# Kernel tuning notes

Measured on AMD Instinct MI355X. Metric: run time of the kernel, lower is better.

The kernel has to match this reference:

```python
import jax, jax.numpy as jnp
import numpy as np

D_MODEL = 1024
NHEAD = 16
HEAD_DIM = D_MODEL // NHEAD


def setup_inputs() -> dict:
    key = jax.random.key(0)
    ks = jax.random.split(key, 9)
    B, T = 2, 2048
    s = 1.0 / np.sqrt(D_MODEL)
    return {
        "sequence": jax.random.normal(ks[0], (B, T, D_MODEL), dtype=jnp.float32),
        "wq": jax.random.normal(ks[1], (D_MODEL, D_MODEL), dtype=jnp.float32) * s,
        "bq": jax.random.normal(ks[2], (D_MODEL,), dtype=jnp.float32) * 0.01,
        "wk": jax.random.normal(ks[3], (D_MODEL, D_MODEL), dtype=jnp.float32) * s,
        "bk": jax.random.normal(ks[4], (D_MODEL,), dtype=jnp.float32) * 0.01,
        "wv": jax.random.normal(ks[5], (D_MODEL, D_MODEL), dtype=jnp.float32) * s,
        "bv": jax.random.normal(ks[6], (D_MODEL,), dtype=jnp.float32) * 0.01,
        "wo": jax.random.normal(ks[7], (D_MODEL, D_MODEL), dtype=jnp.float32) * s,
        "bo": jax.random.normal(ks[8], (D_MODEL,), dtype=jnp.float32) * 0.01,
    }


def reference(sequence, wq, bq, wk, bk, wv, bv, wo, bo):
    B, T, C = sequence.shape
    scale = jnp.asarray(HEAD_DIM ** 0.5, sequence.dtype)
    # projections (nn.Linear: x @ W.T + b)
    def proj(x, w, b):
        y = x @ w.T + b
        return y.reshape(B, T, NHEAD, HEAD_DIM).transpose(0, 2, 1, 3)  # [B,H,T,Dh]
    q = proj(sequence, wq, bq)
    k = proj(sequence, wk, bk)
    v = proj(sequence, wv, bv)
    scores = jnp.einsum("bhqd,bhkd->bhqk", q, k) / scale
    causal = jnp.tril(jnp.ones((T, T), dtype=bool))
    scores = jnp.where(causal, scores, jnp.asarray(-jnp.inf, scores.dtype))
    attn = jax.nn.softmax(scores, axis=-1)
    out = jnp.einsum("bhqk,bhkd->bhqd", attn, v)
    out = out.transpose(0, 2, 1, 3).reshape(B, T, C)
    return out @ wo.T + bo
```

## Files before the change

### kernel.cpp

```cpp
#include <hip/hip_runtime.h>
#include <hip/hip_bf16.h>
#include <hip/hip_fp16.h>
#include <type_traits>

#define DM 1024
#define NH 16
#define HD 64
#define BATCH 2
#define SEQ 2048
#define MROWS (BATCH*SEQ)

typedef __hip_bfloat16 bf16;
typedef __attribute__((ext_vector_type(8))) short    bf16x8;
typedef __attribute__((ext_vector_type(8))) short    s16x8;
typedef __attribute__((ext_vector_type(8))) _Float16 f16x8;
typedef __attribute__((ext_vector_type(4))) _Float16 f16x4;
typedef __attribute__((ext_vector_type(4))) short    s16x4;
typedef __attribute__((ext_vector_type(4))) float    f32x4;

#define LOG2E 1.44269504f
#define M_FIX 4.0f

__device__ __forceinline__ short f2bf(float x) {
    union { float f; unsigned u; } v; v.f = x;
    unsigned r = v.u + 0x7FFF + ((v.u >> 16) & 1);
    return (short)(r >> 16);
}

__device__ __forceinline__ bf16x8 ld8f(const float* p) {
    const float4 a = *(const float4*)p;
    const float4 b = *(const float4*)(p + 4);
    bf16x8 r;
    r[0]=f2bf(a.x); r[1]=f2bf(a.y); r[2]=f2bf(a.z); r[3]=f2bf(a.w);
    r[4]=f2bf(b.x); r[5]=f2bf(b.y); r[6]=f2bf(b.z); r[7]=f2bf(b.w);
    return r;
}

__device__ __forceinline__ void gload_lds16(const void* g, void* l) {
    __builtin_amdgcn_global_load_lds(
        (const __attribute__((address_space(1))) void*)g,
        (__attribute__((address_space(3))) void*)l, 16, 0, 0);
}

__global__ __launch_bounds__(256)
void cvt_bf16(const float* __restrict__ s0, const float* __restrict__ s1,
              const float* __restrict__ s2, const float* __restrict__ s3,
              const float* __restrict__ s4,
              short* d0, short* d1, short* d2, short* d3, short* d4)
{
    const int y = blockIdx.y;
    const float* src = (y==0? s0 : y==1? s1 : y==2? s2 : y==3? s3 : s4);
    short*       dst = (y==0? d0 : y==1? d1 : y==2? d2 : y==3? d3 : d4);
    const int n = (y == 0) ? MROWS*DM : DM*DM;
    const int i = (blockIdx.x * 256 + threadIdx.x) * 8;
    if (i < n) *(bf16x8*)(dst + i) = ld8f(src + i);
}

template<int MODE>
__device__ __forceinline__
void gemm_epilogue(f32x4 (&acc)[4][4], const float* bi, void* out, int z,
                   int tile_m, int tile_n, int wm, int wn,
                   int fr, int quad, int lane, short* lA)
{
    if (MODE == 1 && z == 2) {
        __syncthreads();
        short* sc = lA + (int)(threadIdx.x >> 6) * 256;
        const int rd = lane >> 2, tc = lane & 3;
        #pragma unroll
        for (int mi = 0; mi < 4; ++mi) {
            #pragma unroll
            for (int ni = 0; ni < 4; ++ni) {
                const int colg = tile_n + wn + ni*16 + fr;
                const float bia = bi[colg];
                f16x4 w;
                #pragma unroll
                for (int r = 0; r < 4; ++r) w[r] = (_Float16)(acc[mi][ni][r] + bia);
                *(f16x4*)(sc + fr*16 + quad*4) = w;
                const f16x4 vv = *(const f16x4*)(sc + rd*16 + tc*4);
                const int dg = tile_n + wn + ni*16 + rd;
                const int tg = tile_m + wm + mi*16 + tc*4;
                const int hh = dg >> 6, dd = dg & (HD-1);
                const int bb = tg >> 11, tt = tg & (SEQ-1);
                const int kt = tt >> 5, tko = tt & 31;
                *(f16x4*)((_Float16*)out +
                    ((((size_t)(bb*NH + hh))*(SEQ/32) + kt)*HD + dd)*32 + tko) = vv;
            }
        }
    } else {
        #pragma unroll
        for (int mi = 0; mi < 4; ++mi) {
            #pragma unroll
            for (int ni = 0; ni < 4; ++ni) {
                const int colg = tile_n + wn + ni*16 + fr;
                const float bia = bi[colg];
                #pragma unroll
                for (int r = 0; r < 4; ++r) {
                    const int rowg = tile_m + wm + mi*16 + quad*4 + r;
                    const float v = acc[mi][ni][r] + bia;
                    if (MODE == 0) {
                        ((float*)out)[(size_t)rowg*DM + colg] = v;
                    } else {
                        const int bb = rowg >> 11, t = rowg & (SEQ-1);
                        const int h  = colg >> 6,  d = colg & (HD-1);
                        ((_Float16*)out)[(((size_t)(bb*NH + h))*SEQ + t)*HD + d] = (_Float16)v;
                    }
                }
            }
        }
    }
}

template<int MODE>
__global__ __launch_bounds__(256)
void gemm_a(const short* __restrict__ A,
            const short* __restrict__ W0, const short* __restrict__ W1, const short* __restrict__ W2,
            const float* __restrict__ b0, const float* __restrict__ b1, const float* __restrict__ b2,
            void* o0, void* o1, void* o2)
{
    __shared__ __align__(16) short lA[128*32];
    __shared__ __align__(16) short lB[128*32];

    const int tid  = threadIdx.x;
    const int wid  = tid >> 6;
    const int lane = tid & 63;
    const int tile_n = blockIdx.x * 128;
    const int tile_m = blockIdx.y * 128;
    const int z = blockIdx.z;

    const short* Wg = (z == 0 ? W0 : (z == 1 ? W1 : W2));
    const float* bi = (z == 0 ? b0 : (z == 1 ? b1 : b2));
    void*        out = (z == 0 ? o0 : (z == 1 ? o1 : o2));

    const int sa_row = tile_m + wid*32 + (lane >> 2);
    const int sb_row = tile_n + wid*32 + (lane >> 2);
    const int scol   = (lane & 3) * 8;
    short* lA0 = lA + wid*1024 + lane*8;
    short* lA1 = lA0 + 512;
    short* lB0 = lB + wid*1024 + lane*8;
    short* lB1 = lB0 + 512;

    const int wm = (wid >> 1) * 64;
    const int wn = (wid & 1) * 64;
    const int fr = lane & 15;
    const int quad = lane >> 4;
    const int fq = quad * 8;

    f32x4 acc[4][4] = {};

    for (int k0 = 0; k0 < DM; k0 += 32) {
        __syncthreads();
        gload_lds16(A  + (size_t)sa_row*DM      + k0 + scol, lA0);
        gload_lds16(A  + (size_t)(sa_row+16)*DM + k0 + scol, lA1);
        gload_lds16(Wg + (size_t)sb_row*DM      + k0 + scol, lB0);
        gload_lds16(Wg + (size_t)(sb_row+16)*DM + k0 + scol, lB1);
        __syncthreads();

        bf16x8 af[4], bfv[4];
        #pragma unroll
        for (int i = 0; i < 4; ++i) af[i]  = *(const bf16x8*)(lA + (wm + i*16 + fr)*32 + fq);
        #pragma unroll
        for (int i = 0; i < 4; ++i) bfv[i] = *(const bf16x8*)(lB + (wn + i*16 + fr)*32 + fq);

        #pragma unroll
        for (int mi = 0; mi < 4; ++mi)
            #pragma unroll
            for (int ni = 0; ni < 4; ++ni)
                acc[mi][ni] = __builtin_amdgcn_mfma_f32_16x16x32_bf16(
                    af[mi], bfv[ni], acc[mi][ni], 0, 0, 0);
    }
    gemm_epilogue<MODE>(acc, bi, out, z, tile_m, tile_n, wm, wn, fr, quad, lane, lA);
}

template<typename TA, int MODE>
__global__ __launch_bounds__(256)
void gemm_f(const TA* __restrict__ A,
            const float* __restrict__ W0, const float* __restrict__ W1, const float* __restrict__ W2,
            const float* __restrict__ b0, const float* __restrict__ b1, const float* __restrict__ b2,
            void* o0, void* o1, void* o2)
{
    __shared__ __align__(16) short lA[128*32];
    __shared__ __align__(16) short lB[128*32];

    const int tid  = threadIdx.x;
    const int wid  = tid >> 6;
    const int lane = tid & 63;
    const int tile_n = blockIdx.x * 128;
    const int tile_m = blockIdx.y * 128;
    const int z = blockIdx.z;

    const float* Wg = (z == 0 ? W0 : (z == 1 ? W1 : W2));
    const float* bi = (z == 0 ? b0 : (z == 1 ? b1 : b2));
    void*        out = (z == 0 ? o0 : (z == 1 ? o1 : o2));

    const int sa_row = tile_m + wid*32 + (lane >> 2);
    const int sb_row = tile_n + wid*32 + (lane >> 2);
    const int scol   = (lane & 3) * 8;
    short* lA0 = lA + wid*1024 + lane*8;
    short* lA1 = lA0 + 512;
    short* lB0 = lB + wid*1024 + lane*8;
    short* lB1 = lB0 + 512;

    const int wm = (wid >> 1) * 64;
    const int wn = (wid & 1) * 64;
    const int fr = lane & 15;
    const int quad = lane >> 4;
    const int fq = quad * 8;

    f32x4 acc[4][4] = {};

    for (int k0 = 0; k0 < DM; k0 += 32) {
        bf16x8 ra0, ra1;
        if constexpr (std::is_same<TA, float>::value) {
            ra0 = ld8f((const float*)A + (size_t)sa_row*DM      + k0 + scol);
            ra1 = ld8f((const float*)A + (size_t)(sa_row+16)*DM + k0 + scol);
        } else {
            ra0 = *(const bf16x8*)((const short*)A + (size_t)sa_row*DM      + k0 + scol);
            ra1 = *(const bf16x8*)((const short*)A + (size_t)(sa_row+16)*DM + k0 + scol);
        }
        const bf16x8 rb0 = ld8f(Wg + (size_t)sb_row*DM      + k0 + scol);
        const bf16x8 rb1 = ld8f(Wg + (size_t)(sb_row+16)*DM + k0 + scol);

        __syncthreads();
        *(bf16x8*)lA0 = ra0;
        *(bf16x8*)lA1 = ra1;
        *(bf16x8*)lB0 = rb0;
        *(bf16x8*)lB1 = rb1;
        __syncthreads();

        bf16x8 af[4], bfv[4];
        #pragma unroll
        for (int i = 0; i < 4; ++i) af[i]  = *(const bf16x8*)(lA + (wm + i*16 + fr)*32 + fq);
        #pragma unroll
        for (int i = 0; i < 4; ++i) bfv[i] = *(const bf16x8*)(lB + (wn + i*16 + fr)*32 + fq);

        #pragma unroll
        for (int mi = 0; mi < 4; ++mi)
            #pragma unroll
            for (int ni = 0; ni < 4; ++ni)
                acc[mi][ni] = __builtin_amdgcn_mfma_f32_16x16x32_bf16(
                    af[mi], bfv[ni], acc[mi][ni], 0, 0, 0);
    }
    gemm_epilogue<MODE>(acc, bi, out, z, tile_m, tile_n, wm, wn, fr, quad, lane, lA);
}

__global__ __launch_bounds__(512, 6)
void attn(const _Float16* __restrict__ Q, const _Float16* __restrict__ K,
          const _Float16* __restrict__ Vt, short* __restrict__ O)
{
    __shared__ __align__(16) _Float16 lsK[2][2][2048];
    __shared__ __align__(16) _Float16 lsV[2][2][2048];
    __shared__ __align__(16) float    comb[64*68];
    __shared__ float                  lcomb[64];

    const int t    = threadIdx.x;
    const int lane = t & 63;
    const int wid  = t >> 6;
    const int wg   = wid >> 2;
    const int widl = wid & 3;
    const int tg   = t & 255;
    const int id   = blockIdx.x;
    const int bh   = id & 31;
    const int band = 31 - (id >> 5);
    const size_t base = (size_t)bh * SEQ * HD;
    const int qr = lane & 15;
    const int quad = lane >> 4;
    const int bb = bh >> 4, h = bh & (NH-1);

    const int k_goff = ((tg>>2)&31)*64 + (tg>>7)*32 + (tg&3)*8;
    const int v_goff = (tg&63)*32 + (tg>>6)*8;

    const float SC1 = 0.125f * LOG2E;
    const float SC2 = -M_FIX * LOG2E;
    const int vboff = (quad>>1)*512 + (quad&1)*4 + qr*8;
    const int row   = widl*16 + qr;

    const int q_tile = band*64 + widl*16;
    const int q_idx  = q_tile + qr;
    const int nsub   = band + 1;
    const int k0sub  = wg * nsub;
    const int ktm    = 2*band + (widl >> 1);

    const f16x8* Qv = (const f16x8*)(Q + base + (size_t)q_idx*HD);
    const f16x8 qf0 = Qv[quad];
    const f16x8 qf1 = Qv[quad + 4];

    float l_cur = 0.f;
    f32x4 o[4] = {};

    gload_lds16(K  + base + (size_t)k0sub*2048 + k_goff, &lsK[wg][0][0] + tg*8);
    gload_lds16(Vt + base + (size_t)k0sub*2048 + v_goff, &lsV[wg][0][0] + tg*8);

    int cur = 0;
    #pragma unroll 1
    for (int u = 0; u < nsub; ++u) {
        if (u + 1 < nsub) {
            const size_t g = base + (size_t)(k0sub + u + 1)*2048;
            gload_lds16(K  + g + k_goff, &lsK[wg][cur^1][0] + tg*8);
            gload_lds16(Vt + g + v_goff, &lsV[wg][cur^1][0] + tg*8);
            asm volatile("s_waitcnt vmcnt(2)" ::: "memory");
        } else {
            asm volatile("s_waitcnt vmcnt(0)" ::: "memory");
        }
        __builtin_amdgcn_s_barrier();
        __builtin_amdgcn_sched_barrier(0);

        const int kt32 = k0sub + u;
        if (kt32 <= ktm) {
            const _Float16* sK = &lsK[wg][cur][0];
            const _Float16* sV = &lsV[wg][cur][0];

            const f16x8 ka0 = *(const f16x8*)(sK + qr*32 + quad*8);
            const f16x8 ka1 = *(const f16x8*)(sK + 1024 + qr*32 + quad*8);
            const f16x8 kb0 = *(const f16x8*)(sK + (16+qr)*32 + quad*8);
            const f16x8 kb1 = *(const f16x8*)(sK + 1024 + (16+qr)*32 + quad*8);

            __builtin_amdgcn_s_setprio(1);
            f32x4 s0 = {}, s1 = {};
            s0 = __builtin_amdgcn_mfma_f32_16x16x32_f16(ka0, qf0, s0, 0, 0, 0);
            s0 = __builtin_amdgcn_mfma_f32_16x16x32_f16(ka1, qf1, s0, 0, 0, 0);
            s1 = __builtin_amdgcn_mfma_f32_16x16x32_f16(kb0, qf0, s1, 0, 0, 0);
            s1 = __builtin_amdgcn_mfma_f32_16x16x32_f16(kb1, qf1, s1, 0, 0, 0);

            f16x4 p0, p1;
            const int k_base = kt32*32;
            if (kt32 == ktm) {
                float ls = 0.f;
                #pragma unroll
                for (int r = 0; r < 4; ++r) {
                    const int key = k_base + quad*4 + r;
                    float e0 = exp2f(s0[r] * SC1 + SC2);
                    float e1 = exp2f(s1[r] * SC1 + SC2);
                    e0 = (key      <= q_idx) ? e0 : 0.f;
                    e1 = (key + 16 <= q_idx) ? e1 : 0.f;
                    ls += e0 + e1;
                    p0[r] = (_Float16)e0;
                    p1[r] = (_Float16)e1;
                }
                l_cur += ls;
            } else {
                float ls = 0.f;
                #pragma unroll
                for (int r = 0; r < 4; ++r) {
                    const float e0 = exp2f(s0[r] * SC1 + SC2);
                    const float e1 = exp2f(s1[r] * SC1 + SC2);
                    ls += e0 + e1;
                    p0[r] = (_Float16)e0;
                    p1[r] = (_Float16)e1;
                }
                l_cur += ls;
            }

            #pragma unroll
            for (int dt = 0; dt < 4; ++dt) {
                const f16x4 av0 = *(const f16x4*)(sV + vboff + dt*128);
                const f16x4 av1 = *(const f16x4*)(sV + 1024 + vboff + dt*128);
                o[dt] = __builtin_amdgcn_mfma_f32_16x16x16f16(av0, p0, o[dt], 0, 0, 0);
                o[dt] = __builtin_amdgcn_mfma_f32_16x16x16f16(av1, p1, o[dt], 0, 0, 0);
            }
            __builtin_amdgcn_s_setprio(0);
        }
        __builtin_amdgcn_sched_barrier(0);
        __builtin_amdgcn_s_barrier();
        cur ^= 1;
    }

    l_cur += __shfl_xor(l_cur, 16, 64);
    l_cur += __shfl_xor(l_cur, 32, 64);

    if (wg == 1) {
        #pragma unroll
        for (int dt = 0; dt < 4; ++dt)
            *(f32x4*)&comb[row*68 + dt*16 + quad*4] = o[dt];
        if (quad == 0) lcomb[row] = l_cur;
    }
    __syncthreads();
    if (wg == 0) {
        const float ltot = l_cur + lcomb[row];
        const float linv = 1.0f / fmaxf(ltot, 1e-30f);
        const int tq = q_tile + qr;
        #pragma unroll
        for (int dt = 0; dt < 4; ++dt) {
            const f32x4 o2 = *(const f32x4*)&comb[row*68 + dt*16 + quad*4];
            s16x4 pk;
            #pragma unroll
            for (int r = 0; r < 4; ++r) pk[r] = f2bf((o[dt][r] + o2[r]) * linv);
            *(s16x4*)(O + ((size_t)(bb*SEQ + tq))*DM + h*HD + dt*16 + quad*4) = pk;
        }
    }
}

extern "C" void kernel_launch(void* const* d_in, const int* in_sizes, int n_in,
                              void* d_out, int out_size, void* d_ws, size_t ws_size,
                              hipStream_t stream)
{
    const float* seq = (const float*)d_in[0];
    const float* wq  = (const float*)d_in[1];
    const float* bq  = (const float*)d_in[2];
    const float* wk  = (const float*)d_in[3];
    const float* bk  = (const float*)d_in[4];
    const float* wv  = (const float*)d_in[5];
    const float* bv  = (const float*)d_in[6];
    const float* wo  = (const float*)d_in[7];
    const float* bo  = (const float*)d_in[8];

    _Float16* Qb = (_Float16*)d_ws;
    _Float16* Kb = Qb + (size_t)MROWS*DM;
    _Float16* Vt = Kb + (size_t)MROWS*DM;
    short*    Ob = (short*)(Vt + (size_t)MROWS*DM);
    short*    sq16 = Ob + (size_t)MROWS*DM;
    short*    wq16 = sq16 + (size_t)MROWS*DM;
    short*    wk16 = wq16 + (size_t)DM*DM;
    short*    wv16 = wk16 + (size_t)DM*DM;
    short*    wo16 = wv16 + (size_t)DM*DM;

    const size_t need = ((size_t)MROWS*DM*2)*5 + ((size_t)DM*DM*2)*4;
    const bool fast = ws_size >= need;

    if (fast) {
        dim3 gc(MROWS*DM/(256*8), 5, 1);
        cvt_bf16<<<gc, 256, 0, stream>>>(seq, wq, wk, wv, wo,
                                         sq16, wq16, wk16, wv16, wo16);

        dim3 g1(DM/128, MROWS/128, 3);
        gemm_a<1><<<g1, 256, 0, stream>>>(sq16, wq16, wk16, wv16, bq, bk, bv,
                                          (void*)Qb, (void*)Kb, (void*)Vt);

        attn<<<dim3(1024), 512, 0, stream>>>(Qb, Kb, Vt, Ob);

        dim3 g3(DM/128, MROWS/128, 1);
        gemm_a<0><<<g3, 256, 0, stream>>>(Ob, wo16, wo16, wo16, bo, bo, bo,
                                          d_out, d_out, d_out);
    } else {
        dim3 g1(DM/128, MROWS/128, 3);
        gemm_f<float, 1><<<g1, 256, 0, stream>>>(seq, wq, wk, wv, bq, bk, bv,
                                                 (void*)Qb, (void*)Kb, (void*)Vt);

        attn<<<dim3(1024), 512, 0, stream>>>(Qb, Kb, Vt, Ob);

        dim3 g3(DM/128, MROWS/128, 1);
        gemm_f<short, 0><<<g3, 256, 0, stream>>>(Ob, wo, wo, wo, bo, bo, bo,
                                                 d_out, d_out, d_out);
    }
}
```

Baseline: 186.6 us.

## Load K and V fragments directly from global memory, dropping LDS staging

Removes the double-buffered LDS staging of K and V tiles, along with the per-iteration barriers and waitcnts. Each wave now reads its K and V^T fragments straight from global memory, relying on L2/L1 caching. The loop bound is clipped to the causal end, so waves no longer idle through masked tiles. In exchange, loads are no longer shared across waves through LDS, there is no explicit prefetch, and global loads sit on the critical path right before the MFMAs.

```diff
diff --git a/kernel.cpp b/kernel.cpp
--- a/kernel.cpp
+++ b/kernel.cpp
@@ -247,17 +247,14 @@
 void attn(const _Float16* __restrict__ Q, const _Float16* __restrict__ K,
           const _Float16* __restrict__ Vt, short* __restrict__ O)
 {
-    __shared__ __align__(16) _Float16 lsK[2][2][2048];
-    __shared__ __align__(16) _Float16 lsV[2][2][2048];
-    __shared__ __align__(16) float    comb[64*68];
-    __shared__ float                  lcomb[64];
+    __shared__ __align__(16) float comb[64*68];
+    __shared__ float               lcomb[64];
 
     const int t    = threadIdx.x;
     const int lane = t & 63;
     const int wid  = t >> 6;
     const int wg   = wid >> 2;
     const int widl = wid & 3;
-    const int tg   = t & 255;
     const int id   = blockIdx.x;
     const int bh   = id & 31;
     const int band = 31 - (id >> 5);
@@ -266,12 +263,8 @@
     const int quad = lane >> 4;
     const int bb = bh >> 4, h = bh & (NH-1);
 
-    const int k_goff = ((tg>>2)&31)*64 + (tg>>7)*32 + (tg&3)*8;
-    const int v_goff = (tg&63)*32 + (tg>>6)*8;
-
     const float SC1 = 0.125f * LOG2E;
     const float SC2 = -M_FIX * LOG2E;
-    const int vboff = (quad>>1)*512 + (quad&1)*4 + qr*8;
     const int row   = widl*16 + qr;
 
     const int q_tile = band*64 + widl*16;
@@ -279,89 +272,74 @@
     const int nsub   = band + 1;
     const int k0sub  = wg * nsub;
     const int ktm    = 2*band + (widl >> 1);
+    const int klast  = k0sub + nsub - 1;
+    const int kend   = (ktm < klast) ? ktm : klast;
 
     const f16x8* Qv = (const f16x8*)(Q + base + (size_t)q_idx*HD);
     const f16x8 qf0 = Qv[quad];
     const f16x8 qf1 = Qv[quad + 4];
 
+    const int koff_a = qr*64 + quad*8;
+    const int koff_b = (16 + qr)*64 + quad*8;
+    const int voff   = qr*32 + (quad>>1)*8 + (quad&1)*4;
+
     float l_cur = 0.f;
     f32x4 o[4] = {};
 
-    gload_lds16(K  + base + (size_t)k0sub*2048 + k_goff, &lsK[wg][0][0] + tg*8);
-    gload_lds16(Vt + base + (size_t)k0sub*2048 + v_goff, &lsV[wg][0][0] + tg*8);
-
-    int cur = 0;
     #pragma unroll 1
-    for (int u = 0; u < nsub; ++u) {
-        if (u + 1 < nsub) {
-            const size_t g = base + (size_t)(k0sub + u + 1)*2048;
-            gload_lds16(K  + g + k_goff, &lsK[wg][cur^1][0] + tg*8);
-            gload_lds16(Vt + g + v_goff, &lsV[wg][cur^1][0] + tg*8);
-            asm volatile("s_waitcnt vmcnt(2)" ::: "memory");
+    for (int kt = k0sub; kt <= kend; ++kt) {
+        const _Float16* Kp = K  + base + (size_t)kt*2048;
+        const _Float16* Vp = Vt + base + (size_t)kt*2048;
+
+        const f16x8 ka0 = *(const f16x8*)(Kp + koff_a);
+        const f16x8 ka1 = *(const f16x8*)(Kp + koff_a + 32);
+        const f16x8 kb0 = *(const f16x8*)(Kp + koff_b);
+        const f16x8 kb1 = *(const f16x8*)(Kp + koff_b + 32);
+
+        __builtin_amdgcn_s_setprio(1);
+        f32x4 s0 = {}, s1 = {};
+        s0 = __builtin_amdgcn_mfma_f32_16x16x32_f16(ka0, qf0, s0, 0, 0, 0);
+        s0 = __builtin_amdgcn_mfma_f32_16x16x32_f16(ka1, qf1, s0, 0, 0, 0);
+        s1 = __builtin_amdgcn_mfma_f32_16x16x32_f16(kb0, qf0, s1, 0, 0, 0);
+        s1 = __builtin_amdgcn_mfma_f32_16x16x32_f16(kb1, qf1, s1, 0, 0, 0);
+
+        f16x4 p0, p1;
+        if (kt == ktm) {
+            const int k_base = kt*32;
+            float ls = 0.f;
+            #pragma unroll
+            for (int r = 0; r < 4; ++r) {
+                const int key = k_base + quad*4 + r;
+                float e0 = exp2f(s0[r] * SC1 + SC2);
+                float e1 = exp2f(s1[r] * SC1 + SC2);
+                e0 = (key      <= q_idx) ? e0 : 0.f;
+                e1 = (key + 16 <= q_idx) ? e1 : 0.f;
+                ls += e0 + e1;
+                p0[r] = (_Float16)e0;
+                p1[r] = (_Float16)e1;
+            }
+            l_cur += ls;
         } else {
-            asm volatile("s_waitcnt vmcnt(0)" ::: "memory");
-        }
-        __builtin_amdgcn_s_barrier();
-        __builtin_amdgcn_sched_barrier(0);
-
-        const int kt32 = k0sub + u;
-        if (kt32 <= ktm) {
-            const _Float16* sK = &lsK[wg][cur][0];
-            const _Float16* sV = &lsV[wg][cur][0];
-
-            const f16x8 ka0 = *(const f16x8*)(sK + qr*32 + quad*8);
-            const f16x8 ka1 = *(const f16x8*)(sK + 1024 + qr*32 + quad*8);
-            const f16x8 kb0 = *(const f16x8*)(sK + (16+qr)*32 + quad*8);
-            const f16x8 kb1 = *(const f16x8*)(sK + 1024 + (16+qr)*32 + quad*8);
-
-            __builtin_amdgcn_s_setprio(1);
-            f32x4 s0 = {}, s1 = {};
-            s0 = __builtin_amdgcn_mfma_f32_16x16x32_f16(ka0, qf0, s0, 0, 0, 0);
-            s0 = __builtin_amdgcn_mfma_f32_16x16x32_f16(ka1, qf1, s0, 0, 0, 0);
-            s1 = __builtin_amdgcn_mfma_f32_16x16x32_f16(kb0, qf0, s1, 0, 0, 0);
-            s1 = __builtin_amdgcn_mfma_f32_16x16x32_f16(kb1, qf1, s1, 0, 0, 0);
-
-            f16x4 p0, p1;
-            const int k_base = kt32*32;
-            if (kt32 == ktm) {
-                float ls = 0.f;
-                #pragma unroll
-                for (int r = 0; r < 4; ++r) {
-                    const int key = k_base + quad*4 + r;
-                    float e0 = exp2f(s0[r] * SC1 + SC2);
-                    float e1 = exp2f(s1[r] * SC1 + SC2);
-                    e0 = (key      <= q_idx) ? e0 : 0.f;
-                    e1 = (key + 16 <= q_idx) ? e1 : 0.f;
-                    ls += e0 + e1;
-                    p0[r] = (_Float16)e0;
-                    p1[r] = (_Float16)e1;
-                }
-                l_cur += ls;
-            } else {
-                float ls = 0.f;
-                #pragma unroll
-                for (int r = 0; r < 4; ++r) {
-                    const float e0 = exp2f(s0[r] * SC1 + SC2);
-                    const float e1 = exp2f(s1[r] * SC1 + SC2);
-                    ls += e0 + e1;
-                    p0[r] = (_Float16)e0;
-                    p1[r] = (_Float16)e1;
-                }
-                l_cur += ls;
+            float ls = 0.f;
+            #pragma unroll
+            for (int r = 0; r < 4; ++r) {
+                const float e0 = exp2f(s0[r] * SC1 + SC2);
+                const float e1 = exp2f(s1[r] * SC1 + SC2);
+                ls += e0 + e1;
+                p0[r] = (_Float16)e0;
+                p1[r] = (_Float16)e1;
             }
-
-            #pragma unroll
-            for (int dt = 0; dt < 4; ++dt) {
-                const f16x4 av0 = *(const f16x4*)(sV + vboff + dt*128);
-                const f16x4 av1 = *(const f16x4*)(sV + 1024 + vboff + dt*128);
-                o[dt] = __builtin_amdgcn_mfma_f32_16x16x16f16(av0, p0, o[dt], 0, 0, 0);
-                o[dt] = __builtin_amdgcn_mfma_f32_16x16x16f16(av1, p1, o[dt], 0, 0, 0);
-            }
-            __builtin_amdgcn_s_setprio(0);
-        }
-        __builtin_amdgcn_sched_barrier(0);
-        __builtin_amdgcn_s_barrier();
-        cur ^= 1;
+            l_cur += ls;
+        }
+
+        #pragma unroll
+        for (int dt = 0; dt < 4; ++dt) {
+            const f16x4 av0 = *(const f16x4*)(Vp + voff + dt*512);
+            const f16x4 av1 = *(const f16x4*)(Vp + voff + dt*512 + 16);
+            o[dt] = __builtin_amdgcn_mfma_f32_16x16x16f16(av0, p0, o[dt], 0, 0, 0);
+            o[dt] = __builtin_amdgcn_mfma_f32_16x16x16f16(av1, p1, o[dt], 0, 0, 0);
+        }
+        __builtin_amdgcn_s_setprio(0);
     }
 
     l_cur += __shfl_xor(l_cur, 16, 64);
```

Result: slower. 275.4 us (+47.6%).
